# Optimization experiments

Measured on AMD Instinct MI355X. Metric: run time of the kernel, lower is better.

## Reference

```python
import jax, jax.numpy as jnp
import numpy as np

N_TASK = 50000
N_PROC = 256
N_EDGES = 800000
EMB = 64
HEADS = 4
NLAYERS = 3
EDIM = 8
TDIM = 16
PDIM = 8
NGRAPHS = 8


def setup_inputs():
    key = jax.random.key(0)
    ks = jax.random.split(key, 30)

    def nrm(k, shape, fan_in):
        return jax.random.normal(k, shape, jnp.float32) / np.float32(np.sqrt(fan_in))

    inp = {}
    inp["x_task"] = jax.random.normal(ks[0], (N_TASK, TDIM), jnp.float32)
    inp["x_proc"] = jax.random.normal(ks[1], (N_PROC, PDIM), jnp.float32)
    inp["edge_index"] = jax.random.randint(ks[2], (2, N_EDGES), 0, N_TASK, dtype=jnp.int32)
    inp["edge_attr"] = jax.random.uniform(ks[3], (N_EDGES, EDIM), jnp.float32)
    inp["task_batch"] = jnp.sort(jax.random.randint(ks[4], (N_TASK,), 0, NGRAPHS, dtype=jnp.int32))
    inp["proc_batch"] = jnp.sort(jax.random.randint(ks[5], (N_PROC,), 0, NGRAPHS, dtype=jnp.int32))
    # input embeds
    inp["W_task"] = nrm(ks[6], (TDIM, EMB), TDIM)
    inp["b_task"] = jnp.zeros((EMB,), jnp.float32)
    inp["W_proc"] = nrm(ks[7], (PDIM, EMB), PDIM)
    inp["b_proc"] = jnp.zeros((EMB,), jnp.float32)
    # per-layer GAT params (stacked over layers)
    inp["gat_W"] = nrm(ks[8], (NLAYERS, EMB, HEADS * EMB), EMB)
    inp["gat_We"] = nrm(ks[9], (NLAYERS, EDIM, HEADS * EMB), EDIM)
    inp["att_src"] = nrm(ks[10], (NLAYERS, HEADS, EMB), EMB)
    inp["att_dst"] = nrm(ks[11], (NLAYERS, HEADS, EMB), EMB)
    inp["att_edge"] = nrm(ks[12], (NLAYERS, HEADS, EMB), EMB)
    inp["gat_b"] = jnp.zeros((NLAYERS, HEADS * EMB), jnp.float32)
    inp["proj_W"] = nrm(ks[13], (NLAYERS, HEADS * EMB, EMB), HEADS * EMB)
    inp["proj_b"] = jnp.zeros((NLAYERS, EMB), jnp.float32)
    inp["ln_g"] = jnp.ones((NLAYERS, EMB), jnp.float32)
    inp["ln_b"] = jnp.zeros((NLAYERS, EMB), jnp.float32)
    # heads
    inp["pt_W1"] = nrm(ks[14], (EMB, EMB // 2), EMB)
    inp["pt_b1"] = jnp.zeros((EMB // 2,), jnp.float32)
    inp["pt_W2"] = nrm(ks[15], (EMB // 2, 1), EMB // 2)
    inp["pt_b2"] = jnp.zeros((1,), jnp.float32)
    inp["v_W1"] = nrm(ks[16], (2 * EMB, EMB), 2 * EMB)
    inp["v_b1"] = jnp.zeros((EMB,), jnp.float32)
    inp["v_W2"] = nrm(ks[17], (EMB, 1), EMB)
    inp["v_b2"] = jnp.zeros((1,), jnp.float32)
    return inp


def _gat_layer(x, src, dst, eattr, W, We, a_s, a_d, a_e, bias):
    # PyG GATConv(in=-1 shared lin, heads=H, concat=True, edge_dim) with self loops already appended
    n = x.shape[0]
    xl = (x @ W).reshape(n, HEADS, EMB)            # [N,H,D]
    el = (eattr @ We).reshape(-1, HEADS, EMB)      # [E,H,D]
    a_src = jnp.einsum("nhd,hd->nh", xl, a_s)
    a_dst = jnp.einsum("nhd,hd->nh", xl, a_d)
    a_edg = jnp.einsum("ehd,hd->eh", el, a_e)
    alpha = jax.nn.leaky_relu(a_src[src] + a_dst[dst] + a_edg, 0.2)  # [E,H]
    m = jax.ops.segment_max(alpha, dst, num_segments=n)
    ex = jnp.exp(alpha - m[dst])
    denom = jax.ops.segment_sum(ex, dst, num_segments=n)
    coeff = ex / (denom[dst] + 1e-16)
    out = jax.ops.segment_sum(coeff[:, :, None] * xl[src], dst, num_segments=n)
    return out.reshape(n, HEADS * EMB) + bias


def _mean_pool(x, batch, g):
    s = jax.ops.segment_sum(x, batch, num_segments=g)
    cnt = jax.ops.segment_sum(jnp.ones((x.shape[0], 1), x.dtype), batch, num_segments=g)
    return s / jnp.maximum(cnt, 1.0)


def reference(x_task, x_proc, edge_attr, W_task, b_task, W_proc, b_proc, gat_W, gat_We,
              att_src, att_dst, att_edge, gat_b, proj_W, proj_b, ln_g, ln_b,
              pt_W1, pt_b1, pt_W2, pt_b2, v_W1, v_b1, v_W2, v_b2,
              edge_index, task_batch, proc_batch):
    h_t = x_task @ W_task + b_task
    h_p = x_proc @ W_proc + b_proc
    # add self loops; self-loop edge_attr = mean of edge_attr (PyG fill_value='mean')
    loop = jnp.arange(N_TASK, dtype=edge_index.dtype)
    src = jnp.concatenate([edge_index[0], loop])
    dst = jnp.concatenate([edge_index[1], loop])
    ea = jnp.concatenate([edge_attr, jnp.broadcast_to(edge_attr.mean(0), (N_TASK, EDIM))], axis=0)
    for l in range(NLAYERS):
        upd = _gat_layer(h_t, src, dst, ea, gat_W[l], gat_We[l], att_src[l], att_dst[l], att_edge[l], gat_b[l])
        upd = jax.nn.elu(upd @ proj_W[l] + proj_b[l])
        h = h_t + upd
        mu = h.mean(-1, keepdims=True)
        var = ((h - mu) ** 2).mean(-1, keepdims=True)
        h_t = (h - mu) / jnp.sqrt(var + 1e-5) * ln_g[l] + ln_b[l]
    task_logits = (jax.nn.relu(h_t @ pt_W1 + pt_b1) @ pt_W2 + pt_b2)[:, 0]
    tp = _mean_pool(h_t, task_batch, NGRAPHS)
    pp = _mean_pool(h_p, proc_batch, NGRAPHS)
    ge = jnp.concatenate([tp, pp], axis=1)
    value = jax.nn.relu(ge @ v_W1 + v_b1) @ v_W2 + v_b2
    return task_logits, value, h_t, h_p
```

## Files before the change

### kernel.cpp

```cpp
#include <hip/hip_runtime.h>
#include <hip/hip_bf16.h>
#include <math.h>

#define NT 50000
#define NP 256
#define NE 800000
#define ET 850000
#define EMBD 64
#define NHEADS 4
#define HE 256
#define NG 8
#define NBLK 49

typedef __attribute__((ext_vector_type(8))) short bf16x8;
typedef __attribute__((ext_vector_type(4))) float f32x4;

#define OFF_DEG    0u
#define OFF_INDPTR 200192u
#define OFF_CURSOR 400384u
#define OFF_BLKSUM 600576u
#define OFF_MG     600832u
#define OFF_MH     601216u
#define OFF_MEAN   601280u
#define OFF_TPSUM  601344u
#define OFF_TPCNT  603392u
#define OFF_ER0    603648u
#define OFF_ER1    14203648u
#define OFF_ER2    27803648u
#define OFF_ASRC   41403648u
#define OFF_ADST   42204416u
#define OFF_HT     43005184u
#define OFF_HTB    55817472u
#define OFF_XL     62223616u
#define OFF_AGG    87823616u
#define OFF_WXF    113448192u
#define OFF_WPF    113546496u

__device__ __forceinline__ float bf_lo(unsigned int u) {
  union { unsigned int i; float f; } v; v.i = u << 16; return v.f;
}
__device__ __forceinline__ float bf_hi(unsigned int u) {
  union { unsigned int i; float f; } v; v.i = u & 0xffff0000u; return v.f;
}
__device__ __forceinline__ unsigned pk2(float a, float b) {
  unsigned ua = __bfloat16_as_ushort(__float2bfloat16(a));
  unsigned ub = __bfloat16_as_ushort(__float2bfloat16(b));
  return ua | (ub << 16);
}

__global__ __launch_bounds__(256) void k_embed_task(const float* __restrict__ x,
    const float* __restrict__ W, const float* __restrict__ b,
    float* __restrict__ ht, __hip_bfloat16* __restrict__ htb) {
  int lane = threadIdx.x & 63, wid = threadIdx.x >> 6;
  float breg[16];
  #pragma unroll
  for (int k = 0; k < 16; k++) breg[k] = W[k * 64 + lane];
  float bias = b[lane];
  int row0 = blockIdx.x * 64 + wid * 16;
  #pragma unroll 1
  for (int r = 0; r < 16; r++) {
    int row = row0 + r;
    if (row >= NT) return;
    const float4* xr = (const float4*)(x + (size_t)row * 16);
    float acc = bias;
    #pragma unroll
    for (int q = 0; q < 4; q++) {
      float4 v = xr[q];
      acc += v.x * breg[q*4+0] + v.y * breg[q*4+1] + v.z * breg[q*4+2] + v.w * breg[q*4+3];
    }
    ht[(size_t)row * 64 + lane] = acc;
    htb[(size_t)row * 64 + lane] = __float2bfloat16(acc);
  }
}

__global__ __launch_bounds__(256) void k_degree_mean(const int* __restrict__ ei1,
    const float* __restrict__ ea, int* __restrict__ deg, float* __restrict__ sums) {
  __shared__ float lds[256];
  int tid = threadIdx.x;
  int e = blockIdx.x * 256 + tid;
  if (e < ET) {
    int d = (e < NE) ? ei1[e] : (e - NE);
    atomicAdd(&deg[d], 1);
  }
  int k = tid & 7, rl = tid >> 3;
  float s = 0.f;
  for (int row = blockIdx.x * 32 + rl; row < NE; row += gridDim.x * 32)
    s += ea[(size_t)row * 8 + k];
  lds[tid] = s;
  __syncthreads();
  for (int off = 128; off >= 8; off >>= 1) {
    if (tid < off) lds[tid] += lds[tid + off];
    __syncthreads();
  }
  if (tid < 8) atomicAdd(&sums[tid], lds[tid]);
}

__global__ __launch_bounds__(1024) void k_scanA(const int* __restrict__ deg,
    int* __restrict__ indptr, int* __restrict__ blksum) {
  __shared__ int wsum[16];
  int tid = threadIdx.x, lane = tid & 63, wid = tid >> 6;
  int i = blockIdx.x * 1024 + tid;
  int v = (i < NT) ? deg[i] : 0;
  int x = v;
  #pragma unroll
  for (int off = 1; off < 64; off <<= 1) {
    int t = __shfl_up(x, off, 64);
    if (lane >= off) x += t;
  }
  if (lane == 63) wsum[wid] = x;
  __syncthreads();
  if (wid == 0 && lane < 16) {
    int w = wsum[lane];
    #pragma unroll
    for (int off = 1; off < 16; off <<= 1) {
      int t = __shfl_up(w, off, 64);
      if (lane >= off) w += t;
    }
    wsum[lane] = w;
  }
  __syncthreads();
  int woff = (wid == 0) ? 0 : wsum[wid - 1];
  if (i < NT) indptr[i] = x + woff - v;
  if (tid == 1023) blksum[blockIdx.x] = wsum[15];
}

__global__ __launch_bounds__(1024) void k_scanB(const int* __restrict__ blksum,
    int* __restrict__ indptr, int* __restrict__ cursor) {
  __shared__ int bs[NBLK];
  int tid = threadIdx.x;
  if (tid < NBLK) bs[tid] = blksum[tid];
  __syncthreads();
  int off = 0;
  for (int j = 0; j < (int)blockIdx.x; j++) off += bs[j];
  int i = blockIdx.x * 1024 + tid;
  if (i < NT) {
    int e = indptr[i] + off;
    indptr[i] = e;
    cursor[i] = e;
  }
  if (blockIdx.x == 0 && tid == 0) {
    int tot = 0;
    for (int j = 0; j < NBLK; j++) tot += bs[j];
    indptr[NT] = tot;
  }
}

__global__ __launch_bounds__(128) void k_mprep(const float* __restrict__ We,
    const float* __restrict__ ae, const float* __restrict__ msum,
    float* __restrict__ Mg, float* __restrict__ Mh) {
  int t = threadIdx.x;
  if (t < 96) {
    int l = t >> 5, idx = t & 31, k = idx >> 2, h = idx & 3;
    const float* Wl = We + (size_t)l * 8 * HE;
    const float* al = ae + (size_t)l * NHEADS * EMBD;
    float s = 0.f;
    #pragma unroll
    for (int d = 0; d < 64; d++) s += Wl[k * HE + h * 64 + d] * al[h * 64 + d];
    Mg[t] = s;
  }
  __syncthreads();
  if (t < 12) {
    int l = t >> 2, h = t & 3;
    float m = 0.f;
    #pragma unroll
    for (int k = 0; k < 8; k++) m += msum[k] * (1.f / NE) * Mg[l * 32 + k * 4 + h];
    Mh[t] = m;
  }
}

__global__ __launch_bounds__(256) void k_fill(const int* __restrict__ ei0,
    const int* __restrict__ ei1, const float* __restrict__ ea,
    const float* __restrict__ Mg, const float* __restrict__ Mh,
    int* __restrict__ cursor,
    uint4* __restrict__ er0, uint4* __restrict__ er1, uint4* __restrict__ er2) {
  __shared__ float MgS[96];
  __shared__ float MhS[12];
  int t = threadIdx.x;
  if (t < 96) MgS[t] = Mg[t];
  if (t < 12) MhS[t] = Mh[t];
  __syncthreads();
  int e = blockIdx.x * 256 + t;
  if (e >= ET) return;
  int d, s;
  float r[3][4];
  if (e < NE) {
    d = ei1[e]; s = ei0[e];
    const float4* pp = (const float4*)(ea + (size_t)e * 8);
    float4 v0 = pp[0], v1 = pp[1];
    float v[8] = {v0.x, v0.y, v0.z, v0.w, v1.x, v1.y, v1.z, v1.w};
    #pragma unroll
    for (int l = 0; l < 3; l++) {
      #pragma unroll
      for (int h = 0; h < 4; h++) {
        float acc = 0.f;
        #pragma unroll
        for (int k = 0; k < 8; k++) acc += v[k] * MgS[l * 32 + k * 4 + h];
        r[l][h] = acc;
      }
    }
  } else {
    d = e - NE; s = d;
    #pragma unroll
    for (int l = 0; l < 3; l++)
      #pragma unroll
      for (int h = 0; h < 4; h++) r[l][h] = MhS[l * 4 + h];
  }
  int p = atomicAdd(&cursor[d], 1);
  uint4 rc;
  rc.x = (unsigned)s; rc.w = 0u;
  rc.y = pk2(r[0][0], r[0][1]); rc.z = pk2(r[0][2], r[0][3]); er0[p] = rc;
  rc.y = pk2(r[1][0], r[1][1]); rc.z = pk2(r[1][2], r[1][3]); er1[p] = rc;
  rc.y = pk2(r[2][0], r[2][1]); rc.z = pk2(r[2][2], r[2][3]); er2[p] = rc;
}

__global__ void k_prep_w(const float* __restrict__ Wx, const float* __restrict__ Wp,
                         __hip_bfloat16* __restrict__ Wxf, __hip_bfloat16* __restrict__ Wpf) {
  int lane = threadIdx.x;
  int bid = blockIdx.x;
  int quad = lane >> 4, l15 = lane & 15;
  if (bid < 96) {
    int l = bid >> 5, rem = bid & 31, t = rem >> 1, kb = rem & 1;
    const float* Wl = Wx + (size_t)l * 64 * 256;
    __hip_bfloat16* out = Wxf + (size_t)l * 16384 + (size_t)((t * 2 + kb) * 64 + lane) * 8;
    #pragma unroll
    for (int j = 0; j < 8; j++)
      out[j] = __float2bfloat16(Wl[(kb * 32 + quad * 8 + j) * 256 + t * 16 + l15]);
  } else {
    bid -= 96;
    int l = bid >> 5, rem = bid & 31, t = rem >> 3, kb = rem & 7;
    const float* Wl = Wp + (size_t)l * 256 * 64;
    __hip_bfloat16* out = Wpf + (size_t)l * 16384 + (size_t)((t * 8 + kb) * 64 + lane) * 8;
    #pragma unroll
    for (int j = 0; j < 8; j++)
      out[j] = __float2bfloat16(Wl[(kb * 32 + quad * 8 + j) * 64 + t * 16 + l15]);
  }
}

__global__ __launch_bounds__(256) void k_xl_mfma(
    const __hip_bfloat16* __restrict__ htb, const __hip_bfloat16* __restrict__ Wf,
    const float* __restrict__ as, const float* __restrict__ ad,
    __hip_bfloat16* __restrict__ xl, float* __restrict__ a_src, float* __restrict__ a_dst) {
  __shared__ __hip_bfloat16 cbuf[64 * 264];
  __shared__ float asL[256], adL[256];
  int tid = threadIdx.x;
  int lane = tid & 63, wave = tid >> 6;
  int quad = lane >> 4, l15 = lane & 15;
  asL[tid] = as[tid];
  adL[tid] = ad[tid];
  int r0 = blockIdx.x * 64;
  int arow = r0 + wave * 16 + l15;
  f32x4 acc[16];
  #pragma unroll
  for (int t = 0; t < 16; t++) acc[t] = (f32x4){0.f, 0.f, 0.f, 0.f};
  #pragma unroll
  for (int kb = 0; kb < 2; kb++) {
    bf16x8 a = *(const bf16x8*)(htb + (size_t)arow * 64 + kb * 32 + quad * 8);
    #pragma unroll
    for (int t = 0; t < 16; t++) {
      bf16x8 bfr = *(const bf16x8*)(Wf + (size_t)((t * 2 + kb) * 64 + lane) * 8);
      acc[t] = __builtin_amdgcn_mfma_f32_16x16x32_bf16(a, bfr, acc[t], 0, 0, 0);
    }
  }
  int rloc = wave * 16 + quad * 4;
  #pragma unroll
  for (int t = 0; t < 16; t++) {
    #pragma unroll
    for (int reg = 0; reg < 4; reg++)
      cbuf[(rloc + reg) * 264 + t * 16 + l15] = __float2bfloat16(acc[t][reg]);
  }
  __syncthreads();
  {
    int r = tid & 63, q = tid >> 6;
    const __hip_bfloat16* rowp = &cbuf[r * 264 + q * 64];
    float vs = 0.f, vd = 0.f;
    #pragma unroll
    for (int d8 = 0; d8 < 8; d8++) {
      uint4 u = *(const uint4*)(rowp + d8 * 8);
      float x0 = bf_lo(u.x), x1 = bf_hi(u.x), x2 = bf_lo(u.y), x3 = bf_hi(u.y);
      float x4 = bf_lo(u.z), x5 = bf_hi(u.z), x6 = bf_lo(u.w), x7 = bf_hi(u.w);
      const float* ap = &asL[q * 64 + d8 * 8];
      const float* dp = &adL[q * 64 + d8 * 8];
      vs += x0*ap[0]+x1*ap[1]+x2*ap[2]+x3*ap[3]+x4*ap[4]+x5*ap[5]+x6*ap[6]+x7*ap[7];
      vd += x0*dp[0]+x1*dp[1]+x2*dp[2]+x3*dp[3]+x4*dp[4]+x5*dp[5]+x6*dp[6]+x7*dp[7];
    }
    int row = r0 + r;
    if (row < NT) {
      a_src[row * 4 + q] = vs;
      a_dst[row * 4 + q] = vd;
    }
  }
  #pragma unroll
  for (int k = 0; k < 8; k++) {
    int c = k * 256 + tid;
    int row = c >> 5, off = c & 31;
    if (r0 + row < NT) {
      uint4 v = *(const uint4*)(&cbuf[row * 264 + off * 8]);
      *(uint4*)(xl + (size_t)(r0 + row) * HE + off * 8) = v;
    }
  }
}

__global__ __launch_bounds__(256) void k_attn(
    const __hip_bfloat16* __restrict__ xl, const float* __restrict__ a_src,
    const float* __restrict__ a_dst, const uint4* __restrict__ er,
    const int* __restrict__ indptr, const float* __restrict__ gb,
    __hip_bfloat16* __restrict__ agg) {
  int node = blockIdx.x * 4 + (threadIdx.x >> 6);
  int lane = threadIdx.x & 63;
  int h = lane >> 4;
  int hbase = lane & 48;
  int e15 = lane & 15;
  int beg = indptr[node], end = indptr[node + 1];
  float adh = a_dst[node * 4 + h];
  float M = -1e30f, S = 0.f;
  float acc0 = 0.f, acc1 = 0.f, acc2 = 0.f, acc3 = 0.f;
  for (int base = beg; base < end; base += 16) {
    int cnt = min(16, end - base);
    bool ok = e15 < cnt;
    uint4 rec; rec.x = 0u; rec.y = 0u; rec.z = 0u; rec.w = 0u;
    if (ok) rec = er[base + e15];
    int my_src = (int)rec.x;
    unsigned wsel = (h < 2) ? rec.y : rec.z;
    float aeh = (h & 1) ? bf_hi(wsel) : bf_lo(wsel);
    float asr = ok ? a_src[(size_t)my_src * 4 + h] : 0.f;
    float al = asr + adh + aeh;
    al = (al > 0.f) ? al : 0.2f * al;
    if (!ok) al = -1e30f;
    float cm = al;
    #pragma unroll
    for (int off = 1; off < 16; off <<= 1) cm = fmaxf(cm, __shfl_xor(cm, off, 64));
    float newM = fmaxf(M, cm);
    float corr = __expf(M - newM);
    float ex = __expf(al - newM);
    float cs = ex;
    #pragma unroll
    for (int off = 1; off < 16; off <<= 1) cs += __shfl_xor(cs, off, 64);
    S = S * corr + cs;
    M = newM;
    acc0 *= corr; acc1 *= corr; acc2 *= corr; acc3 *= corr;
    if (cnt == 16) {
      #pragma unroll 4
      for (int j = 0; j < 16; j++) {
        int src = __shfl(my_src, j, 64);
        float cf = __shfl(ex, hbase | j, 64);
        uint2 u = *(const uint2*)(xl + (size_t)src * HE + lane * 4);
        acc0 += cf * bf_lo(u.x);
        acc1 += cf * bf_hi(u.x);
        acc2 += cf * bf_lo(u.y);
        acc3 += cf * bf_hi(u.y);
      }
    } else {
      for (int j = 0; j < cnt; j++) {
        int src = __shfl(my_src, j, 64);
        float cf = __shfl(ex, hbase | j, 64);
        uint2 u = *(const uint2*)(xl + (size_t)src * HE + lane * 4);
        acc0 += cf * bf_lo(u.x);
        acc1 += cf * bf_hi(u.x);
        acc2 += cf * bf_lo(u.y);
        acc3 += cf * bf_hi(u.y);
      }
    }
  }
  float inv = 1.f / (S + 1e-16f);
  float4 g4 = *(const float4*)(gb + lane * 4);
  unsigned int o0 = __bfloat16_as_ushort(__float2bfloat16(acc0 * inv + g4.x));
  unsigned int o1 = __bfloat16_as_ushort(__float2bfloat16(acc1 * inv + g4.y));
  unsigned int o2 = __bfloat16_as_ushort(__float2bfloat16(acc2 * inv + g4.z));
  unsigned int o3 = __bfloat16_as_ushort(__float2bfloat16(acc3 * inv + g4.w));
  uint2 out; out.x = o0 | (o1 << 16); out.y = o2 | (o3 << 16);
  *(uint2*)(agg + (size_t)node * HE + lane * 4) = out;
}

__global__ __launch_bounds__(256) void k_proj_mfma(
    const __hip_bfloat16* __restrict__ agg, const __hip_bfloat16* __restrict__ Wf,
    const float* __restrict__ pb, const float* __restrict__ g, const float* __restrict__ b,
    const float* __restrict__ ht_in, float* __restrict__ ht_out,
    __hip_bfloat16* __restrict__ htb_out, int writebf) {
  __shared__ float cbuf[64 * 68];
  __shared__ float red[8 * 64];
  __shared__ float stats[2 * 64];
  __shared__ float pbL[64], gL[64], bL[64];
  int tid = threadIdx.x;
  int lane = tid & 63, wave = tid >> 6;
  int quad = lane >> 4, l15 = lane & 15;
  if (tid < 64) { pbL[tid] = pb[tid]; gL[tid] = g[tid]; bL[tid] = b[tid]; }
  int r0 = blockIdx.x * 64;
  int arow = r0 + wave * 16 + l15;
  f32x4 acc[4];
  #pragma unroll
  for (int t = 0; t < 4; t++) acc[t] = (f32x4){0.f, 0.f, 0.f, 0.f};
  #pragma unroll
  for (int kb = 0; kb < 8; kb++) {
    bf16x8 a = *(const bf16x8*)(agg + (size_t)arow * HE + kb * 32 + quad * 8);
    #pragma unroll
    for (int t = 0; t < 4; t++) {
      bf16x8 bfr = *(const bf16x8*)(Wf + (size_t)((t * 8 + kb) * 64 + lane) * 8);
      acc[t] = __builtin_amdgcn_mfma_f32_16x16x32_bf16(a, bfr, acc[t], 0, 0, 0);
    }
  }
  int rloc = wave * 16 + quad * 4;
  #pragma unroll
  for (int t = 0; t < 4; t++) {
    #pragma unroll
    for (int reg = 0; reg < 4; reg++)
      cbuf[(rloc + reg) * 68 + t * 16 + l15] = acc[t][reg];
  }
  __syncthreads();
  int r = tid >> 2, q = tid & 3;
  int row = r0 + r;
  float h[16];
  float s1 = 0.f, s2 = 0.f;
  const float* hin = ht_in + (size_t)row * 64 + q * 16;
  #pragma unroll
  for (int d = 0; d < 16; d++) {
    float u = cbuf[r * 68 + q * 16 + d] + pbL[q * 16 + d];
    u = (u > 0.f) ? u : (__expf(u) - 1.f);
    float hv = hin[d] + u;
    h[d] = hv;
    s1 += hv; s2 += hv * hv;
  }
  red[q * 64 + r] = s1;
  red[256 + q * 64 + r] = s2;
  __syncthreads();
  if (tid < 64) {
    float sa = red[tid] + red[64 + tid] + red[128 + tid] + red[192 + tid];
    float sb = red[256 + tid] + red[320 + tid] + red[384 + tid] + red[448 + tid];
    float mu = sa * 0.015625f;
    float var = sb * 0.015625f - mu * mu;
    stats[tid] = mu;
    stats[64 + tid] = rsqrtf(var + 1e-5f);
  }
  __syncthreads();
  float mu = stats[r], rstd = stats[64 + r];
  if (row < NT) {
    float o[16];
    #pragma unroll
    for (int d = 0; d < 16; d++)
      o[d] = (h[d] - mu) * rstd * gL[q * 16 + d] + bL[q * 16 + d];
    float* outp = ht_out + (size_t)row * 64 + q * 16;
    #pragma unroll
    for (int d4 = 0; d4 < 4; d4++) {
      float4 v; v.x = o[d4*4]; v.y = o[d4*4+1]; v.z = o[d4*4+2]; v.w = o[d4*4+3];
      *(float4*)(outp + d4 * 4) = v;
    }
    if (writebf) {
      uint4 u0, u1;
      u0.x = pk2(o[0], o[1]);  u0.y = pk2(o[2], o[3]);
      u0.z = pk2(o[4], o[5]);  u0.w = pk2(o[6], o[7]);
      u1.x = pk2(o[8], o[9]);  u1.y = pk2(o[10], o[11]);
      u1.z = pk2(o[12], o[13]); u1.w = pk2(o[14], o[15]);
      uint4* hb = (uint4*)(htb_out + (size_t)row * 64 + q * 16);
      hb[0] = u0; hb[1] = u1;
    }
  }
}

__global__ __launch_bounds__(256) void k_task_head(const float* __restrict__ ht,
    const float* __restrict__ W1, const float* __restrict__ b1,
    const float* __restrict__ W2, const float* __restrict__ b2, float* __restrict__ logits) {
  __shared__ float lh[8 * 64];
  int t = threadIdx.x;
  size_t base = (size_t)blockIdx.x * 8 * 64;
  lh[t] = ht[base + t];
  lh[t + 256] = ht[base + t + 256];
  __syncthreads();
  int i = t >> 5, j = t & 31;
  float s = b1[j];
  #pragma unroll 8
  for (int d = 0; d < 64; d++) s += lh[i * 64 + d] * W1[d * 32 + j];
  s = fmaxf(s, 0.f);
  float p = s * W2[j];
  #pragma unroll
  for (int off = 16; off; off >>= 1) p += __shfl_xor(p, off, 64);
  if (j == 0) logits[blockIdx.x * 8 + i] = p + b2[0];
}

__global__ __launch_bounds__(256) void k_pool_task(const float* __restrict__ ht,
    const int* __restrict__ tb, float* __restrict__ sums, float* __restrict__ cnt) {
  int lane = threadIdx.x & 63, sub = threadIdx.x >> 6;
  float acc[8], c[8];
  #pragma unroll
  for (int g = 0; g < 8; g++) { acc[g] = 0.f; c[g] = 0.f; }
  int lim = min(NT, (int)((blockIdx.x + 1) * 512));
  for (int n = blockIdx.x * 512 + sub; n < lim; n += 4) {
    int g = tb[n];
    float v = ht[(size_t)n * 64 + lane];
    #pragma unroll
    for (int gg = 0; gg < 8; gg++) {
      if (g == gg) { acc[gg] += v; c[gg] += 1.f; }
    }
  }
  #pragma unroll
  for (int g = 0; g < 8; g++) {
    if (__any(acc[g] != 0.f || c[g] != 0.f)) {
      atomicAdd(&sums[g * 64 + lane], acc[g]);
      if (lane == 0) atomicAdd(&cnt[g], c[g]);
    }
  }
}

__global__ __launch_bounds__(512) void k_value(const float* __restrict__ tpsum,
    const float* __restrict__ tpcnt, const float* __restrict__ x_proc,
    const float* __restrict__ W_proc, const float* __restrict__ b_proc,
    float* __restrict__ hp_out, const int* __restrict__ pbatch,
    const float* __restrict__ vW1, const float* __restrict__ vb1,
    const float* __restrict__ vW2, const float* __restrict__ vb2,
    float* __restrict__ val_out) {
  __shared__ float ge[8 * 128];
  int t = threadIdx.x;
  int g = t >> 6, d = t & 63;
  float wreg[8];
  #pragma unroll
  for (int k = 0; k < 8; k++) wreg[k] = W_proc[k * 64 + d];
  float bd = b_proc[d];
  for (int p = g; p < 256; p += 8) {
    const float* xr = x_proc + (size_t)p * 8;
    float a = bd;
    #pragma unroll
    for (int k = 0; k < 8; k++) a += xr[k] * wreg[k];
    hp_out[(size_t)p * 64 + d] = a;
  }
  __syncthreads();
  float c = fmaxf(tpcnt[g], 1.f);
  ge[g * 128 + d] = tpsum[g * 64 + d] / c;
  float s = 0.f, cc = 0.f;
  for (int p = 0; p < 256; p++) {
    int bg = pbatch[p];
    if (bg == g) { s += hp_out[(size_t)p * 64 + d]; cc += 1.f; }
  }
  ge[g * 128 + 64 + d] = s / fmaxf(cc, 1.f);
  __syncthreads();
  float acc = vb1[d];
  #pragma unroll 8
  for (int k = 0; k < 128; k++) acc += ge[g * 128 + k] * vW1[k * 64 + d];
  acc = fmaxf(acc, 0.f);
  float p = acc * vW2[d];
  #pragma unroll
  for (int off = 32; off; off >>= 1) p += __shfl_xor(p, off, 64);
  if (d == 0) val_out[g] = p + vb2[0];
}

extern "C" void kernel_launch(void* const* d_in, const int* in_sizes, int n_in,
                              void* d_out, int out_size, void* d_ws, size_t ws_size,
                              hipStream_t stream) {
  (void)in_sizes; (void)n_in; (void)out_size; (void)ws_size;
  const float* x_task  = (const float*)d_in[0];
  const float* x_proc  = (const float*)d_in[1];
  const int*   eidx    = (const int*)d_in[2];
  const float* eattr   = (const float*)d_in[3];
  const int*   tbatch  = (const int*)d_in[4];
  const int*   pbatch  = (const int*)d_in[5];
  const float* W_task  = (const float*)d_in[6];
  const float* b_task  = (const float*)d_in[7];
  const float* W_proc  = (const float*)d_in[8];
  const float* b_proc  = (const float*)d_in[9];
  const float* gat_W   = (const float*)d_in[10];
  const float* gat_We  = (const float*)d_in[11];
  const float* att_src = (const float*)d_in[12];
  const float* att_dst = (const float*)d_in[13];
  const float* att_edge= (const float*)d_in[14];
  const float* gat_b   = (const float*)d_in[15];
  const float* proj_W  = (const float*)d_in[16];
  const float* proj_b  = (const float*)d_in[17];
  const float* ln_g    = (const float*)d_in[18];
  const float* ln_b    = (const float*)d_in[19];
  const float* pt_W1   = (const float*)d_in[20];
  const float* pt_b1   = (const float*)d_in[21];
  const float* pt_W2   = (const float*)d_in[22];
  const float* pt_b2   = (const float*)d_in[23];
  const float* v_W1    = (const float*)d_in[24];
  const float* v_b1    = (const float*)d_in[25];
  const float* v_W2    = (const float*)d_in[26];
  const float* v_b2    = (const float*)d_in[27];

  char* ws = (char*)d_ws;
  int*   deg    = (int*)(ws + OFF_DEG);
  int*   indptr = (int*)(ws + OFF_INDPTR);
  int*   cursor = (int*)(ws + OFF_CURSOR);
  int*   blksum = (int*)(ws + OFF_BLKSUM);
  float* Mg     = (float*)(ws + OFF_MG);
  float* Mh     = (float*)(ws + OFF_MH);
  float* msum   = (float*)(ws + OFF_MEAN);
  float* tpsum  = (float*)(ws + OFF_TPSUM);
  float* tpcnt  = (float*)(ws + OFF_TPCNT);
  uint4* er0    = (uint4*)(ws + OFF_ER0);
  uint4* er1    = (uint4*)(ws + OFF_ER1);
  uint4* er2    = (uint4*)(ws + OFF_ER2);
  float* a_src  = (float*)(ws + OFF_ASRC);
  float* a_dst  = (float*)(ws + OFF_ADST);
  float* ht     = (float*)(ws + OFF_HT);
  __hip_bfloat16* htb = (__hip_bfloat16*)(ws + OFF_HTB);
  __hip_bfloat16* xl  = (__hip_bfloat16*)(ws + OFF_XL);
  __hip_bfloat16* agg = (__hip_bfloat16*)(ws + OFF_AGG);
  __hip_bfloat16* wxf = (__hip_bfloat16*)(ws + OFF_WXF);
  __hip_bfloat16* wpf = (__hip_bfloat16*)(ws + OFF_WPF);
  uint4* ers[3] = {er0, er1, er2};

  float* out_logits = (float*)d_out;
  float* out_value  = (float*)d_out + NT;
  float* out_ht     = (float*)d_out + NT + NG;
  float* out_hp     = (float*)d_out + NT + NG + (size_t)NT * EMBD;

  hipMemsetAsync(ws + OFF_DEG, 0, NT * 4, stream);
  hipMemsetAsync(ws + OFF_MEAN, 0, 2144, stream);

  k_embed_task<<<782, 256, 0, stream>>>(x_task, W_task, b_task, ht, htb);
  k_degree_mean<<<(ET + 255) / 256, 256, 0, stream>>>(eidx + NE, eattr, deg, msum);
  k_scanA<<<NBLK, 1024, 0, stream>>>(deg, indptr, blksum);
  k_scanB<<<NBLK, 1024, 0, stream>>>(blksum, indptr, cursor);
  k_mprep<<<1, 128, 0, stream>>>(gat_We, att_edge, msum, Mg, Mh);
  k_fill<<<(ET + 255) / 256, 256, 0, stream>>>(eidx, eidx + NE, eattr, Mg, Mh,
                                               cursor, er0, er1, er2);
  k_prep_w<<<192, 64, 0, stream>>>(gat_W, proj_W, wxf, wpf);

  for (int l = 0; l < 3; l++) {
    k_xl_mfma<<<782, 256, 0, stream>>>(htb, wxf + (size_t)l * 16384,
                                       att_src + l * NHEADS * EMBD,
                                       att_dst + l * NHEADS * EMBD,
                                       xl, a_src, a_dst);
    k_attn<<<NT / 4, 256, 0, stream>>>(xl, a_src, a_dst, ers[l], indptr,
                                       gat_b + l * HE, agg);
    float* htout = (l == 2) ? out_ht : ht;
    k_proj_mfma<<<782, 256, 0, stream>>>(agg, wpf + (size_t)l * 16384,
                                         proj_b + l * EMBD, ln_g + l * EMBD,
                                         ln_b + l * EMBD, ht, htout, htb,
                                         (l == 2) ? 0 : 1);
  }

  k_task_head<<<NT / 8, 256, 0, stream>>>(out_ht, pt_W1, pt_b1, pt_W2, pt_b2, out_logits);
  k_pool_task<<<(NT + 511) / 512, 256, 0, stream>>>(out_ht, tbatch, tpsum, tpcnt);
  k_value<<<1, 512, 0, stream>>>(tpsum, tpcnt, x_proc, W_proc, b_proc, out_hp,
                                 pbatch, v_W1, v_b1, v_W2, v_b2, out_value);
}
```

Measured before the change: 694.6 us.

## Fuse embed and proj with next-layer xl GEMM, fold attention dots into MFMA

Merges the task embedding into the first xl GEMM kernel, and fuses each layer's projection+layernorm with the next layer's xl GEMM. This removes the bf16 h_t round trip and a kernel launch per layer. The per-head src/dst attention dot products are precomputed into a folded weight (W·a), so a_src/a_dst come from one extra MFMA instead of an LDS reduction. The layernorm row reduction now uses shuffles instead of shared memory and syncs. In exchange, a_src/a_dst are computed from bf16-rounded folded weights, which slightly changes numerics, and the fused kernel uses more shared memory and registers.

```diff
diff --git a/kernel.cpp b/kernel.cpp
--- a/kernel.cpp
+++ b/kernel.cpp
@@ -30,11 +30,11 @@
 #define OFF_ASRC   41403648u
 #define OFF_ADST   42204416u
 #define OFF_HT     43005184u
-#define OFF_HTB    55817472u
-#define OFF_XL     62223616u
-#define OFF_AGG    87823616u
-#define OFF_WXF    113448192u
-#define OFF_WPF    113546496u
+#define OFF_XL     55817472u
+#define OFF_AGG    81417472u
+#define OFF_WXF    107042048u
+#define OFF_WPF    107140352u
+#define OFF_WSD    107238656u
 
 __device__ __forceinline__ float bf_lo(unsigned int u) {
   union { unsigned int i; float f; } v; v.i = u << 16; return v.f;
@@ -46,31 +46,6 @@
   unsigned ua = __bfloat16_as_ushort(__float2bfloat16(a));
   unsigned ub = __bfloat16_as_ushort(__float2bfloat16(b));
   return ua | (ub << 16);
-}
-
-__global__ __launch_bounds__(256) void k_embed_task(const float* __restrict__ x,
-    const float* __restrict__ W, const float* __restrict__ b,
-    float* __restrict__ ht, __hip_bfloat16* __restrict__ htb) {
-  int lane = threadIdx.x & 63, wid = threadIdx.x >> 6;
-  float breg[16];
-  #pragma unroll
-  for (int k = 0; k < 16; k++) breg[k] = W[k * 64 + lane];
-  float bias = b[lane];
-  int row0 = blockIdx.x * 64 + wid * 16;
-  #pragma unroll 1
-  for (int r = 0; r < 16; r++) {
-    int row = row0 + r;
-    if (row >= NT) return;
-    const float4* xr = (const float4*)(x + (size_t)row * 16);
-    float acc = bias;
-    #pragma unroll
-    for (int q = 0; q < 4; q++) {
-      float4 v = xr[q];
-      acc += v.x * breg[q*4+0] + v.y * breg[q*4+1] + v.z * breg[q*4+2] + v.w * breg[q*4+3];
-    }
-    ht[(size_t)row * 64 + lane] = acc;
-    htb[(size_t)row * 64 + lane] = __float2bfloat16(acc);
-  }
 }
 
 __global__ __launch_bounds__(256) void k_degree_mean(const int* __restrict__ ei1,
@@ -145,9 +120,11 @@
   }
 }
 
-__global__ __launch_bounds__(128) void k_mprep(const float* __restrict__ We,
+__global__ __launch_bounds__(256) void k_mprep(const float* __restrict__ We,
     const float* __restrict__ ae, const float* __restrict__ msum,
-    float* __restrict__ Mg, float* __restrict__ Mh) {
+    const float* __restrict__ Wx, const float* __restrict__ as_all,
+    const float* __restrict__ ad_all,
+    float* __restrict__ Mg, float* __restrict__ Mh, __hip_bfloat16* __restrict__ wsd) {
   int t = threadIdx.x;
   if (t < 96) {
     int l = t >> 5, idx = t & 31, k = idx >> 2, h = idx & 3;
@@ -165,6 +142,22 @@
     #pragma unroll
     for (int k = 0; k < 8; k++) m += msum[k] * (1.f / NE) * Mg[l * 32 + k * 4 + h];
     Mh[t] = m;
+  }
+  for (int v = t; v < 3072; v += 256) {
+    int l = v >> 10, rem = v & 1023;
+    int kb = rem >> 9, rem2 = rem & 511;
+    int lane = rem2 >> 3, j = rem2 & 7;
+    int quad = lane >> 4, l15 = lane & 15;
+    int k = kb * 32 + quad * 8 + j;
+    float val = 0.f;
+    if (l15 < 8) {
+      int h = l15 & 3;
+      const float* av = ((l15 < 4) ? as_all : ad_all) + (size_t)l * NHEADS * EMBD + h * 64;
+      const float* Wr = Wx + (size_t)l * 64 * 256 + (size_t)k * 256 + h * 64;
+      #pragma unroll
+      for (int d = 0; d < 64; d++) val += Wr[d] * av[d];
+    }
+    wsd[(size_t)l * 1024 + (size_t)(kb * 64 + lane) * 8 + j] = __float2bfloat16(val);
   }
 }
 
@@ -236,65 +229,75 @@
   }
 }
 
-__global__ __launch_bounds__(256) void k_xl_mfma(
-    const __hip_bfloat16* __restrict__ htb, const __hip_bfloat16* __restrict__ Wf,
-    const float* __restrict__ as, const float* __restrict__ ad,
-    __hip_bfloat16* __restrict__ xl, float* __restrict__ a_src, float* __restrict__ a_dst) {
-  __shared__ __hip_bfloat16 cbuf[64 * 264];
-  __shared__ float asL[256], adL[256];
-  int tid = threadIdx.x;
-  int lane = tid & 63, wave = tid >> 6;
+__global__ __launch_bounds__(256) void k_embed_xl(const float* __restrict__ x,
+    const float* __restrict__ W, const float* __restrict__ b,
+    const __hip_bfloat16* __restrict__ Wf, const __hip_bfloat16* __restrict__ wsd,
+    float* __restrict__ ht, __hip_bfloat16* __restrict__ xl,
+    float* __restrict__ a_src, float* __restrict__ a_dst) {
+  __shared__ __hip_bfloat16 hbuf[64 * 72];
+  __shared__ __hip_bfloat16 cb16[64 * 264];
+  int tid = threadIdx.x, lane = tid & 63, wave = tid >> 6;
   int quad = lane >> 4, l15 = lane & 15;
-  asL[tid] = as[tid];
-  adL[tid] = ad[tid];
   int r0 = blockIdx.x * 64;
-  int arow = r0 + wave * 16 + l15;
-  f32x4 acc[16];
+  {
+    float breg[16];
+    #pragma unroll
+    for (int k = 0; k < 16; k++) breg[k] = W[k * 64 + lane];
+    float bias = b[lane];
+    #pragma unroll 1
+    for (int rr = 0; rr < 16; rr++) {
+      int row = r0 + wave * 16 + rr;
+      float acc = bias;
+      if (row < NT) {
+        const float4* xr = (const float4*)(x + (size_t)row * 16);
+        #pragma unroll
+        for (int q = 0; q < 4; q++) {
+          float4 v = xr[q];
+          acc += v.x * breg[q*4+0] + v.y * breg[q*4+1] + v.z * breg[q*4+2] + v.w * breg[q*4+3];
+        }
+        ht[(size_t)row * 64 + lane] = acc;
+      }
+      hbuf[(wave * 16 + rr) * 72 + lane] = __float2bfloat16(acc);
+    }
+  }
+  __syncthreads();
+  f32x4 acc[16], accE;
   #pragma unroll
   for (int t = 0; t < 16; t++) acc[t] = (f32x4){0.f, 0.f, 0.f, 0.f};
+  accE = (f32x4){0.f, 0.f, 0.f, 0.f};
   #pragma unroll
   for (int kb = 0; kb < 2; kb++) {
-    bf16x8 a = *(const bf16x8*)(htb + (size_t)arow * 64 + kb * 32 + quad * 8);
+    bf16x8 a = *(const bf16x8*)(&hbuf[(wave * 16 + l15) * 72 + kb * 32 + quad * 8]);
     #pragma unroll
     for (int t = 0; t < 16; t++) {
       bf16x8 bfr = *(const bf16x8*)(Wf + (size_t)((t * 2 + kb) * 64 + lane) * 8);
       acc[t] = __builtin_amdgcn_mfma_f32_16x16x32_bf16(a, bfr, acc[t], 0, 0, 0);
     }
+    bf16x8 bs = *(const bf16x8*)(wsd + (size_t)(kb * 64 + lane) * 8);
+    accE = __builtin_amdgcn_mfma_f32_16x16x32_bf16(a, bs, accE, 0, 0, 0);
   }
   int rloc = wave * 16 + quad * 4;
   #pragma unroll
   for (int t = 0; t < 16; t++) {
     #pragma unroll
     for (int reg = 0; reg < 4; reg++)
-      cbuf[(rloc + reg) * 264 + t * 16 + l15] = __float2bfloat16(acc[t][reg]);
-  }
-  __syncthreads();
-  {
-    int r = tid & 63, q = tid >> 6;
-    const __hip_bfloat16* rowp = &cbuf[r * 264 + q * 64];
-    float vs = 0.f, vd = 0.f;
-    #pragma unroll
-    for (int d8 = 0; d8 < 8; d8++) {
-      uint4 u = *(const uint4*)(rowp + d8 * 8);
-      float x0 = bf_lo(u.x), x1 = bf_hi(u.x), x2 = bf_lo(u.y), x3 = bf_hi(u.y);
-      float x4 = bf_lo(u.z), x5 = bf_hi(u.z), x6 = bf_lo(u.w), x7 = bf_hi(u.w);
-      const float* ap = &asL[q * 64 + d8 * 8];
-      const float* dp = &adL[q * 64 + d8 * 8];
-      vs += x0*ap[0]+x1*ap[1]+x2*ap[2]+x3*ap[3]+x4*ap[4]+x5*ap[5]+x6*ap[6]+x7*ap[7];
-      vd += x0*dp[0]+x1*dp[1]+x2*dp[2]+x3*dp[3]+x4*dp[4]+x5*dp[5]+x6*dp[6]+x7*dp[7];
-    }
-    int row = r0 + r;
-    if (row < NT) {
-      a_src[row * 4 + q] = vs;
-      a_dst[row * 4 + q] = vd;
-    }
-  }
+      cb16[(rloc + reg) * 264 + t * 16 + l15] = __float2bfloat16(acc[t][reg]);
+  }
+  #pragma unroll
+  for (int reg = 0; reg < 4; reg++) {
+    int row = r0 + rloc + reg;
+    if (l15 < 8 && row < NT) {
+      float* dst = (l15 < 4) ? a_src : a_dst;
+      dst[row * 4 + (l15 & 3)] = accE[reg];
+    }
+  }
+  __syncthreads();
   #pragma unroll
   for (int k = 0; k < 8; k++) {
     int c = k * 256 + tid;
     int row = c >> 5, off = c & 31;
     if (r0 + row < NT) {
-      uint4 v = *(const uint4*)(&cbuf[row * 264 + off * 8]);
+      uint4 v = *(const uint4*)(&cb16[row * 264 + off * 8]);
       *(uint4*)(xl + (size_t)(r0 + row) * HE + off * 8) = v;
     }
   }
@@ -371,31 +374,146 @@
   *(uint2*)(agg + (size_t)node * HE + lane * 4) = out;
 }
 
-__global__ __launch_bounds__(256) void k_proj_mfma(
-    const __hip_bfloat16* __restrict__ agg, const __hip_bfloat16* __restrict__ Wf,
-    const float* __restrict__ pb, const float* __restrict__ g, const float* __restrict__ b,
-    const float* __restrict__ ht_in, float* __restrict__ ht_out,
-    __hip_bfloat16* __restrict__ htb_out, int writebf) {
-  __shared__ float cbuf[64 * 68];
-  __shared__ float red[8 * 64];
-  __shared__ float stats[2 * 64];
+__global__ __launch_bounds__(256) void k_proj_xl(
+    const __hip_bfloat16* __restrict__ agg, const __hip_bfloat16* __restrict__ Wpf,
+    const float* __restrict__ pb, const float* __restrict__ g, const float* __restrict__ bln,
+    const float* __restrict__ ht_io,
+    const __hip_bfloat16* __restrict__ Wxf, const __hip_bfloat16* __restrict__ wsd,
+    float* __restrict__ ht_out, __hip_bfloat16* __restrict__ xl,
+    float* __restrict__ a_src, float* __restrict__ a_dst) {
+  __shared__ __hip_bfloat16 cb16[64 * 264];
+  __shared__ __hip_bfloat16 hbuf[64 * 72];
   __shared__ float pbL[64], gL[64], bL[64];
-  int tid = threadIdx.x;
-  int lane = tid & 63, wave = tid >> 6;
+  float* cbf = (float*)cb16;
+  int tid = threadIdx.x, lane = tid & 63, wave = tid >> 6;
   int quad = lane >> 4, l15 = lane & 15;
-  if (tid < 64) { pbL[tid] = pb[tid]; gL[tid] = g[tid]; bL[tid] = b[tid]; }
+  if (tid < 64) { pbL[tid] = pb[tid]; gL[tid] = g[tid]; bL[tid] = bln[tid]; }
   int r0 = blockIdx.x * 64;
   int arow = r0 + wave * 16 + l15;
-  f32x4 acc[4];
-  #pragma unroll
-  for (int t = 0; t < 4; t++) acc[t] = (f32x4){0.f, 0.f, 0.f, 0.f};
+  {
+    f32x4 pacc[4];
+    #pragma unroll
+    for (int t = 0; t < 4; t++) pacc[t] = (f32x4){0.f, 0.f, 0.f, 0.f};
+    #pragma unroll
+    for (int kb = 0; kb < 8; kb++) {
+      bf16x8 a = *(const bf16x8*)(agg + (size_t)arow * HE + kb * 32 + quad * 8);
+      #pragma unroll
+      for (int t = 0; t < 4; t++) {
+        bf16x8 bfr = *(const bf16x8*)(Wpf + (size_t)((t * 8 + kb) * 64 + lane) * 8);
+        pacc[t] = __builtin_amdgcn_mfma_f32_16x16x32_bf16(a, bfr, pacc[t], 0, 0, 0);
+      }
+    }
+    int rloc = wave * 16 + quad * 4;
+    #pragma unroll
+    for (int t = 0; t < 4; t++) {
+      #pragma unroll
+      for (int reg = 0; reg < 4; reg++)
+        cbf[(rloc + reg) * 68 + t * 16 + l15] = pacc[t][reg];
+    }
+  }
+  __syncthreads();
+  {
+    int r = tid >> 2, q = tid & 3;
+    int row = r0 + r;
+    float h[16], s1 = 0.f, s2 = 0.f;
+    const float* hin = ht_io + (size_t)row * 64 + q * 16;
+    #pragma unroll
+    for (int d = 0; d < 16; d++) {
+      float u = cbf[r * 68 + q * 16 + d] + pbL[q * 16 + d];
+      u = (u > 0.f) ? u : (__expf(u) - 1.f);
+      float hv = hin[d] + u;
+      h[d] = hv;
+      s1 += hv; s2 += hv * hv;
+    }
+    s1 += __shfl_xor(s1, 1, 64); s1 += __shfl_xor(s1, 2, 64);
+    s2 += __shfl_xor(s2, 1, 64); s2 += __shfl_xor(s2, 2, 64);
+    float mu = s1 * 0.015625f;
+    float var = s2 * 0.015625f - mu * mu;
+    float rstd = rsqrtf(var + 1e-5f);
+    float o[16];
+    #pragma unroll
+    for (int d = 0; d < 16; d++)
+      o[d] = (h[d] - mu) * rstd * gL[q * 16 + d] + bL[q * 16 + d];
+    if (row < NT) {
+      float* outp = ht_out + (size_t)row * 64 + q * 16;
+      #pragma unroll
+      for (int d4 = 0; d4 < 4; d4++) {
+        float4 v; v.x = o[d4*4]; v.y = o[d4*4+1]; v.z = o[d4*4+2]; v.w = o[d4*4+3];
+        *(float4*)(outp + d4 * 4) = v;
+      }
+    }
+    uint4 u0, u1;
+    u0.x = pk2(o[0], o[1]);  u0.y = pk2(o[2], o[3]);
+    u0.z = pk2(o[4], o[5]);  u0.w = pk2(o[6], o[7]);
+    u1.x = pk2(o[8], o[9]);  u1.y = pk2(o[10], o[11]);
+    u1.z = pk2(o[12], o[13]); u1.w = pk2(o[14], o[15]);
+    uint4* hb = (uint4*)(&hbuf[r * 72 + q * 16]);
+    hb[0] = u0; hb[1] = u1;
+  }
+  __syncthreads();
+  f32x4 acc[16], accE;
+  #pragma unroll
+  for (int t = 0; t < 16; t++) acc[t] = (f32x4){0.f, 0.f, 0.f, 0.f};
+  accE = (f32x4){0.f, 0.f, 0.f, 0.f};
+  #pragma unroll
+  for (int kb = 0; kb < 2; kb++) {
+    bf16x8 a = *(const bf16x8*)(&hbuf[(wave * 16 + l15) * 72 + kb * 32 + quad * 8]);
+    #pragma unroll
+    for (int t = 0; t < 16; t++) {
+      bf16x8 bfr = *(const bf16x8*)(Wxf + (size_t)((t * 2 + kb) * 64 + lane) * 8);
+      acc[t] = __builtin_amdgcn_mfma_f32_16x16x32_bf16(a, bfr, acc[t], 0, 0, 0);
+    }
+    bf16x8 bs = *(const bf16x8*)(wsd + (size_t)(kb * 64 + lane) * 8);
+    accE = __builtin_amdgcn_mfma_f32_16x16x32_bf16(a, bs, accE, 0, 0, 0);
+  }
+  int rloc = wave * 16 + quad * 4;
+  #pragma unroll
+  for (int t = 0; t < 16; t++) {
+    #pragma unroll
+    for (int reg = 0; reg < 4; reg++)
+      cb16[(rloc + reg) * 264 + t * 16 + l15] = __float2bfloat16(acc[t][reg]);
+  }
+  #pragma unroll
+  for (int reg = 0; reg < 4; reg++) {
+    int row = r0 + rloc + reg;
+    if (l15 < 8 && row < NT) {
+      float* dst = (l15 < 4) ? a_src : a_dst;
+      dst[row * 4 + (l15 & 3)] = accE[reg];
+    }
+  }
+  __syncthreads();
+  #pragma unroll
+  for (int k = 0; k < 8; k++) {
+    int c = k * 256 + tid;
+    int row = c >> 5, off = c & 31;
+    if (r0 + row < NT) {
+      uint4 v = *(const uint4*)(&cb16[row * 264 + off * 8]);
+      *(uint4*)(xl + (size_t)(r0 + row) * HE + off * 8) = v;
+    }
+  }
+}
+
+__global__ __launch_bounds__(256) void k_proj_last(
+    const __hip_bfloat16* __restrict__ agg, const __hip_bfloat16* __restrict__ Wpf,
+    const float* __restrict__ pb, const float* __restrict__ g, const float* __restrict__ bln,
+    const float* __restrict__ ht_in, float* __restrict__ ht_out) {
+  __shared__ float cbf[64 * 68];
+  __shared__ float pbL[64], gL[64], bL[64];
+  int tid = threadIdx.x, lane = tid & 63, wave = tid >> 6;
+  int quad = lane >> 4, l15 = lane & 15;
+  if (tid < 64) { pbL[tid] = pb[tid]; gL[tid] = g[tid]; bL[tid] = bln[tid]; }
+  int r0 = blockIdx.x * 64;
+  int arow = r0 + wave * 16 + l15;
+  f32x4 pacc[4];
+  #pragma unroll
+  for (int t = 0; t < 4; t++) pacc[t] = (f32x4){0.f, 0.f, 0.f, 0.f};
   #pragma unroll
   for (int kb = 0; kb < 8; kb++) {
     bf16x8 a = *(const bf16x8*)(agg + (size_t)arow * HE + kb * 32 + quad * 8);
     #pragma unroll
     for (int t = 0; t < 4; t++) {
-      bf16x8 bfr = *(const bf16x8*)(Wf + (size_t)((t * 8 + kb) * 64 + lane) * 8);
-      acc[t] = __builtin_amdgcn_mfma_f32_16x16x32_bf16(a, bfr, acc[t], 0, 0, 0);
+      bf16x8 bfr = *(const bf16x8*)(Wpf + (size_t)((t * 8 + kb) * 64 + lane) * 8);
+      pacc[t] = __builtin_amdgcn_mfma_f32_16x16x32_bf16(a, bfr, pacc[t], 0, 0, 0);
     }
   }
   int rloc = wave * 16 + quad * 4;
@@ -403,54 +521,36 @@
   for (int t = 0; t < 4; t++) {
     #pragma unroll
     for (int reg = 0; reg < 4; reg++)
-      cbuf[(rloc + reg) * 68 + t * 16 + l15] = acc[t][reg];
+      cbf[(rloc + reg) * 68 + t * 16 + l15] = pacc[t][reg];
   }
   __syncthreads();
   int r = tid >> 2, q = tid & 3;
   int row = r0 + r;
-  float h[16];
-  float s1 = 0.f, s2 = 0.f;
+  float h[16], s1 = 0.f, s2 = 0.f;
   const float* hin = ht_in + (size_t)row * 64 + q * 16;
   #pragma unroll
   for (int d = 0; d < 16; d++) {
-    float u = cbuf[r * 68 + q * 16 + d] + pbL[q * 16 + d];
+    float u = cbf[r * 68 + q * 16 + d] + pbL[q * 16 + d];
     u = (u > 0.f) ? u : (__expf(u) - 1.f);
     float hv = hin[d] + u;
     h[d] = hv;
     s1 += hv; s2 += hv * hv;
   }
-  red[q * 64 + r] = s1;
-  red[256 + q * 64 + r] = s2;
-  __syncthreads();
-  if (tid < 64) {
-    float sa = red[tid] + red[64 + tid] + red[128 + tid] + red[192 + tid];
-    float sb = red[256 + tid] + red[320 + tid] + red[384 + tid] + red[448 + tid];
-    float mu = sa * 0.015625f;
-    float var = sb * 0.015625f - mu * mu;
-    stats[tid] = mu;
-    stats[64 + tid] = rsqrtf(var + 1e-5f);
-  }
-  __syncthreads();
-  float mu = stats[r], rstd = stats[64 + r];
+  s1 += __shfl_xor(s1, 1, 64); s1 += __shfl_xor(s1, 2, 64);
+  s2 += __shfl_xor(s2, 1, 64); s2 += __shfl_xor(s2, 2, 64);
+  float mu = s1 * 0.015625f;
+  float var = s2 * 0.015625f - mu * mu;
+  float rstd = rsqrtf(var + 1e-5f);
   if (row < NT) {
-    float o[16];
-    #pragma unroll
-    for (int d = 0; d < 16; d++)
-      o[d] = (h[d] - mu) * rstd * gL[q * 16 + d] + bL[q * 16 + d];
     float* outp = ht_out + (size_t)row * 64 + q * 16;
     #pragma unroll
     for (int d4 = 0; d4 < 4; d4++) {
-      float4 v; v.x = o[d4*4]; v.y = o[d4*4+1]; v.z = o[d4*4+2]; v.w = o[d4*4+3];
+      float4 v;
+      v.x = (h[d4*4+0] - mu) * rstd * gL[q*16+d4*4+0] + bL[q*16+d4*4+0];
+      v.y = (h[d4*4+1] - mu) * rstd * gL[q*16+d4*4+1] + bL[q*16+d4*4+1];
+      v.z = (h[d4*4+2] - mu) * rstd * gL[q*16+d4*4+2] + bL[q*16+d4*4+2];
+      v.w = (h[d4*4+3] - mu) * rstd * gL[q*16+d4*4+3] + bL[q*16+d4*4+3];
       *(float4*)(outp + d4 * 4) = v;
-    }
-    if (writebf) {
-      uint4 u0, u1;
-      u0.x = pk2(o[0], o[1]);  u0.y = pk2(o[2], o[3]);
-      u0.z = pk2(o[4], o[5]);  u0.w = pk2(o[6], o[7]);
-      u1.x = pk2(o[8], o[9]);  u1.y = pk2(o[10], o[11]);
-      u1.z = pk2(o[12], o[13]); u1.w = pk2(o[14], o[15]);
-      uint4* hb = (uint4*)(htb_out + (size_t)row * 64 + q * 16);
-      hb[0] = u0; hb[1] = u1;
     }
   }
 }
@@ -589,11 +689,11 @@
   float* a_src  = (float*)(ws + OFF_ASRC);
   float* a_dst  = (float*)(ws + OFF_ADST);
   float* ht     = (float*)(ws + OFF_HT);
-  __hip_bfloat16* htb = (__hip_bfloat16*)(ws + OFF_HTB);
   __hip_bfloat16* xl  = (__hip_bfloat16*)(ws + OFF_XL);
   __hip_bfloat16* agg = (__hip_bfloat16*)(ws + OFF_AGG);
   __hip_bfloat16* wxf = (__hip_bfloat16*)(ws + OFF_WXF);
   __hip_bfloat16* wpf = (__hip_bfloat16*)(ws + OFF_WPF);
+  __hip_bfloat16* wsd = (__hip_bfloat16*)(ws + OFF_WSD);
   uint4* ers[3] = {er0, er1, er2};
 
   float* out_logits = (float*)d_out;
@@ -604,27 +704,32 @@
   hipMemsetAsync(ws + OFF_DEG, 0, NT * 4, stream);
   hipMemsetAsync(ws + OFF_MEAN, 0, 2144, stream);
 
-  k_embed_task<<<782, 256, 0, stream>>>(x_task, W_task, b_task, ht, htb);
   k_degree_mean<<<(ET + 255) / 256, 256, 0, stream>>>(eidx + NE, eattr, deg, msum);
   k_scanA<<<NBLK, 1024, 0, stream>>>(deg, indptr, blksum);
   k_scanB<<<NBLK, 1024, 0, stream>>>(blksum, indptr, cursor);
-  k_mprep<<<1, 128, 0, stream>>>(gat_We, att_edge, msum, Mg, Mh);
+  k_mprep<<<1, 256, 0, stream>>>(gat_We, att_edge, msum, gat_W, att_src, att_dst,
+                                 Mg, Mh, wsd);
+  k_prep_w<<<192, 64, 0, stream>>>(gat_W, proj_W, wxf, wpf);
   k_fill<<<(ET + 255) / 256, 256, 0, stream>>>(eidx, eidx + NE, eattr, Mg, Mh,
                                                cursor, er0, er1, er2);
-  k_prep_w<<<192, 64, 0, stream>>>(gat_W, proj_W, wxf, wpf);
+  k_embed_xl<<<782, 256, 0, stream>>>(x_task, W_task, b_task, wxf, wsd,
+                                      ht, xl, a_src, a_dst);
 
   for (int l = 0; l < 3; l++) {
-    k_xl_mfma<<<782, 256, 0, stream>>>(htb, wxf + (size_t)l * 16384,
-                                       att_src + l * NHEADS * EMBD,
-                                       att_dst + l * NHEADS * EMBD,
-                                       xl, a_src, a_dst);
     k_attn<<<NT / 4, 256, 0, stream>>>(xl, a_src, a_dst, ers[l], indptr,
                                        gat_b + l * HE, agg);
-    float* htout = (l == 2) ? out_ht : ht;
-    k_proj_mfma<<<782, 256, 0, stream>>>(agg, wpf + (size_t)l * 16384,
+    if (l < 2) {
+      k_proj_xl<<<782, 256, 0, stream>>>(agg, wpf + (size_t)l * 16384,
                                          proj_b + l * EMBD, ln_g + l * EMBD,
-                                         ln_b + l * EMBD, ht, htout, htb,
-                                         (l == 2) ? 0 : 1);
+                                         ln_b + l * EMBD, ht,
+                                         wxf + (size_t)(l + 1) * 16384,
+                                         wsd + (size_t)(l + 1) * 1024,
+                                         ht, xl, a_src, a_dst);
+    } else {
+      k_proj_last<<<782, 256, 0, stream>>>(agg, wpf + (size_t)l * 16384,
+                                           proj_b + l * EMBD, ln_g + l * EMBD,
+                                           ln_b + l * EMBD, ht, out_ht);
+    }
   }
 
   k_task_head<<<NT / 8, 256, 0, stream>>>(out_ht, pt_W1, pt_b1, pt_W2, pt_b2, out_logits);
```

Result: no change. 684.7 us (-1.4%).
